# Kernel optimization log

Measured on AMD Instinct MI355X. Metric: run time of the kernel, lower is better.

The kernel has to match this reference:

```python
import jax, jax.numpy as jnp
import numpy as np

NBITS = 4
OUT_F = 2048
IN_F = 2048


def _bit_ste(w, nbits):
    # clamp to [-1,1], quantize magnitude to nbits levels, keep sign
    step = float(2 ** nbits - 1)
    w = jnp.clip(w, -1.0, 1.0)
    return jnp.round(jnp.abs(w) * step) / step * jnp.sign(w)


def setup_inputs() -> dict:
    key = jax.random.key(0)
    ks = jax.random.split(key, 6)
    ex = np.arange(NBITS - 1, -1, -1)
    exps = jnp.asarray(2.0 ** ex / (2.0 ** NBITS - 1), dtype=jnp.float32)
    inp = {
        "input": jax.random.normal(ks[0], (8, 2048, IN_F), dtype=jnp.float32),
        # bit-plane weights: sigmoid of these gives soft bits in (0,1)
        "pweight": jax.random.normal(ks[1], (OUT_F, IN_F, NBITS), dtype=jnp.float32),
        "nweight": jax.random.normal(ks[2], (OUT_F, IN_F, NBITS), dtype=jnp.float32),
        "exps": exps,
        "bexps": exps,
        "mask_weight": jnp.ones((NBITS,), dtype=jnp.float32),  # init.constant_(1)
        "scale": jnp.array([0.05], dtype=jnp.float32),
        "pbias": jax.random.uniform(ks[3], (OUT_F, NBITS), dtype=jnp.float32, minval=0.0, maxval=float(2 ** NBITS - 1)) // 1.0 % 2.0,
        "nbias": jax.random.uniform(ks[4], (OUT_F, NBITS), dtype=jnp.float32, minval=0.0, maxval=float(2 ** NBITS - 1)) // 1.0 % 2.0,
        "biasscale": jnp.array([0.05], dtype=jnp.float32),
    }
    return inp


def reference(input, pweight, nweight, exps, bexps, mask_weight, scale, pbias, nbias, biasscale):
    temp = 1.0
    # temp_s and mask_discrete are all-ones buffers -> identity factors
    mask = jax.nn.sigmoid(mask_weight)                      # [N]
    soft = jax.nn.sigmoid(temp * pweight) - jax.nn.sigmoid(temp * nweight)  # [O,I,N]
    weight = jnp.einsum('oin,n->oi', soft, exps * mask) * scale[0]          # [O,I]
    bias_raw = jnp.einsum('on,n->o', pbias - nbias, bexps)  # [O]
    bias = _bit_ste(bias_raw, NBITS) * biasscale[0]
    # F.linear: y = x @ W^T + b
    return jnp.einsum('bsi,oi->bso', input, weight) + bias
```

## Files before the change

kernel.cpp:

```cpp
#include <hip/hip_runtime.h>
#include <hip/hip_bf16.h>
#include <stdint.h>

#define M_DIM 16384
#define N_DIM 2048
#define K_DIM 2048

typedef __attribute__((ext_vector_type(8))) __bf16 bf16x8;
typedef __attribute__((ext_vector_type(4))) float f32x4;

__device__ __forceinline__ unsigned short f2bf(float f) {
  unsigned int u = __builtin_bit_cast(unsigned int, f);
  u += 0x7FFFu + ((u >> 16) & 1u);
  return (unsigned short)(u >> 16);
}

__device__ __forceinline__ float sigmoidf_(float x) {
  return 1.0f / (1.0f + __expf(-x));
}

__global__ __launch_bounds__(256) void convert_x(const float4* __restrict__ x,
                                                 uint4* __restrict__ xb) {
  int idx = blockIdx.x * 256 + threadIdx.x;
  float4 a = x[idx * 2];
  float4 b = x[idx * 2 + 1];
  uint4 r;
  r.x = (unsigned)f2bf(a.x) | ((unsigned)f2bf(a.y) << 16);
  r.y = (unsigned)f2bf(a.z) | ((unsigned)f2bf(a.w) << 16);
  r.z = (unsigned)f2bf(b.x) | ((unsigned)f2bf(b.y) << 16);
  r.w = (unsigned)f2bf(b.z) | ((unsigned)f2bf(b.w) << 16);
  xb[idx] = r;
}

__global__ __launch_bounds__(256) void make_w(const float4* __restrict__ pw,
                                              const float4* __restrict__ nw,
                                              const float* __restrict__ exps,
                                              const float* __restrict__ maskw,
                                              const float* __restrict__ scale,
                                              unsigned short* __restrict__ wout) {
  int idx = blockIdx.x * 256 + threadIdx.x;
  float4 p = pw[idx];
  float4 n = nw[idx];
  float s = scale[0];
  float c0 = sigmoidf_(maskw[0]) * exps[0] * s;
  float c1 = sigmoidf_(maskw[1]) * exps[1] * s;
  float c2 = sigmoidf_(maskw[2]) * exps[2] * s;
  float c3 = sigmoidf_(maskw[3]) * exps[3] * s;
  float w = (sigmoidf_(p.x) - sigmoidf_(n.x)) * c0
          + (sigmoidf_(p.y) - sigmoidf_(n.y)) * c1
          + (sigmoidf_(p.z) - sigmoidf_(n.z)) * c2
          + (sigmoidf_(p.w) - sigmoidf_(n.w)) * c3;
  wout[idx] = f2bf(w);
}

__global__ __launch_bounds__(256) void make_bias(const float* __restrict__ pb,
                                                 const float* __restrict__ nb,
                                                 const float* __restrict__ bexps,
                                                 const float* __restrict__ bscale,
                                                 float* __restrict__ bias) {
  int o = blockIdx.x * 256 + threadIdx.x;
  if (o < N_DIM) {
    float x = 0.f;
#pragma unroll
    for (int n = 0; n < 4; ++n) x += (pb[o * 4 + n] - nb[o * 4 + n]) * bexps[n];
    float xc = fminf(fmaxf(x, -1.f), 1.f);
    float mag = rintf(fabsf(xc) * 15.f) * (1.f / 15.f);
    float sgn = (xc > 0.f) ? 1.f : ((xc < 0.f) ? -1.f : 0.f);
    bias[o] = mag * sgn * bscale[0];
  }
}


#define BM 256
#define BN 256
#define BK 64
#define NT (K_DIM / BK)

__device__ __forceinline__ void gload16(const void* g, void* l) {
  __builtin_amdgcn_global_load_lds(
      (const __attribute__((address_space(1))) unsigned int*)g,
      (__attribute__((address_space(3))) unsigned int*)l, 16, 0, 0);
}

#define VMCNT(n) asm volatile("s_waitcnt vmcnt(" #n ")" ::: "memory")
#define BAR() __builtin_amdgcn_s_barrier()

__global__ __launch_bounds__(512, 2) void gemm_bias(const unsigned short* __restrict__ X,
                                                    const unsigned short* __restrict__ W,
                                                    const float* __restrict__ bias,
                                                    float* __restrict__ out) {
  __shared__ unsigned short sA[2][BM * BK];
  __shared__ unsigned short sB[2][BN * BK];

  const int tid = threadIdx.x;
  const int swz = ((int)blockIdx.x & 7) * 64 + ((int)blockIdx.x >> 3);
  const int bm = swz >> 3;
  const int bn = swz & 7;
  const int row0 = bm * BM, col0 = bn * BN;

  const int w = tid >> 6, l = tid & 63;
  const int wr = w >> 2;
  const int wc = w & 3;
  const int lr = l & 15;
  const int lk4 = l >> 4;
  const int l7 = l & 7;

  const unsigned short* Ag = X + (size_t)row0 * K_DIM;
  const unsigned short* Bg = W + (size_t)col0 * K_DIM;

  const int srl = (tid >> 3) & 31;
  const int sc16 = (tid & 7) ^ ((tid >> 3) & 7);
  const int shi = tid >> 8;
  const int slin = ((tid >> 3) & 24) * 64 + (tid & 63) * 8;

  auto stage = [&](unsigned short* lbase, const unsigned short* gbase,
                   int rb0, int rb1, int tk) {
    int rb = shi ? rb1 : rb0;
    int trow = rb + srl;
    gload16(gbase + (size_t)trow * K_DIM + tk * BK + sc16 * 8,
            lbase + rb * 64 + slin);
  };

  auto rdA = [&](const unsigned short* base, int mf, int ks) -> bf16x8 {
    int trow = wr * 128 + mf * 16 + lr;
    int c16l = (ks * 4 + lk4) ^ l7;
    return *(const bf16x8*)&base[trow * 64 + c16l * 8];
  };
  auto rdB = [&](const unsigned short* base, int nf, int ks) -> bf16x8 {
    int trow = wc * 64 + nf * 16 + lr;
    int c16l = (ks * 4 + lk4) ^ l7;
    return *(const bf16x8*)&base[trow * 64 + c16l * 8];
  };

  f32x4 acc[8][4] = {};
  bf16x8 a[4][2], b[4][2];

#define PHASE_MFMA(mh, nh)                                                    \
  __builtin_amdgcn_s_setprio(1);                                              \
  _Pragma("unroll") for (int i = 0; i < 4; ++i)                               \
  _Pragma("unroll") for (int j = 0; j < 2; ++j)                               \
  _Pragma("unroll") for (int ks = 0; ks < 2; ++ks)                            \
      acc[(mh) * 4 + i][(nh) * 2 + j] = __builtin_amdgcn_mfma_f32_16x16x32_bf16( \
          a[i][ks], b[(nh) * 2 + j][ks], acc[(mh) * 4 + i][(nh) * 2 + j], 0, 0, 0); \
  __builtin_amdgcn_s_setprio(0);

  {
    unsigned short* qa = sA[0];
    unsigned short* qb = sB[0];
    stage(qa, Ag, 0, 32, 0);
    stage(qa, Ag, 128, 160, 0);
    stage(qb, Bg, 0, 64, 0);
    stage(qb, Bg, 128, 192, 0);
    stage(qb, Bg, 32, 96, 0);
    stage(qb, Bg, 160, 224, 0);
    stage(qa, Ag, 64, 96, 0);
    stage(qa, Ag, 192, 224, 0);
  }
  VMCNT(4);
  BAR();

  for (int t = 0; t < NT; ++t) {
    const int p = t & 1, q = p ^ 1;
    const bool last = (t == NT - 1);
    const unsigned short* pa = sA[p];
    const unsigned short* pb = sB[p];
    unsigned short* qa = sA[q];
    unsigned short* qb = sB[q];

#pragma unroll
    for (int i = 0; i < 4; ++i)
#pragma unroll
      for (int ks = 0; ks < 2; ++ks) a[i][ks] = rdA(pa, i, ks);
#pragma unroll
    for (int j = 0; j < 2; ++j)
#pragma unroll
      for (int ks = 0; ks < 2; ++ks) b[j][ks] = rdB(pb, j, ks);
    if (!last) { stage(qa, Ag, 0, 32, t + 1); stage(qa, Ag, 128, 160, t + 1); }
    BAR();
    PHASE_MFMA(0, 0);
    if (!last) { VMCNT(4); } else { VMCNT(2); }
    BAR();

#pragma unroll
    for (int j = 2; j < 4; ++j)
#pragma unroll
      for (int ks = 0; ks < 2; ++ks) b[j][ks] = rdB(pb, j, ks);
    if (!last) { stage(qb, Bg, 0, 64, t + 1); stage(qb, Bg, 128, 192, t + 1); }
    BAR();
    PHASE_MFMA(0, 1);
    if (!last) { VMCNT(4); } else { VMCNT(0); }
    BAR();

#pragma unroll
    for (int i = 0; i < 4; ++i)
#pragma unroll
      for (int ks = 0; ks < 2; ++ks) a[i][ks] = rdA(pa, 4 + i, ks);
    if (!last) { stage(qb, Bg, 32, 96, t + 1); stage(qb, Bg, 160, 224, t + 1); }
    BAR();
    PHASE_MFMA(1, 0);
    BAR();

    if (!last) { stage(qa, Ag, 64, 96, t + 1); stage(qa, Ag, 192, 224, t + 1); }
    BAR();
    PHASE_MFMA(1, 1);
    if (!last) { VMCNT(4); }
    BAR();
  }

  float bv[4];
#pragma unroll
  for (int nf = 0; nf < 4; ++nf) bv[nf] = bias[col0 + wc * 64 + nf * 16 + lr];
  const int orow = lk4 * 4;
#pragma unroll
  for (int mf = 0; mf < 8; ++mf) {
#pragma unroll
    for (int nf = 0; nf < 4; ++nf) {
      const int colg = col0 + wc * 64 + nf * 16 + lr;
#pragma unroll
      for (int r = 0; r < 4; ++r) {
        int rowg = row0 + wr * 128 + mf * 16 + orow + r;
        out[(size_t)rowg * N_DIM + colg] = acc[mf][nf][r] + bv[nf];
      }
    }
  }
#undef PHASE_MFMA
}

extern "C" void kernel_launch(void* const* d_in, const int* in_sizes, int n_in,
                              void* d_out, int out_size, void* d_ws, size_t ws_size,
                              hipStream_t stream) {
  const float* input  = (const float*)d_in[0];
  const float* pweight = (const float*)d_in[1];
  const float* nweight = (const float*)d_in[2];
  const float* exps   = (const float*)d_in[3];
  const float* bexps  = (const float*)d_in[4];
  const float* maskw  = (const float*)d_in[5];
  const float* scale  = (const float*)d_in[6];
  const float* pbias  = (const float*)d_in[7];
  const float* nbias  = (const float*)d_in[8];
  const float* bscale = (const float*)d_in[9];
  float* out = (float*)d_out;

  unsigned short* Xb = (unsigned short*)d_ws;
  unsigned short* Wb = (unsigned short*)((char*)d_ws + (size_t)M_DIM * K_DIM * 2);
  float* bias = (float*)((char*)d_ws + (size_t)M_DIM * K_DIM * 2 + (size_t)N_DIM * K_DIM * 2);

  convert_x<<<(M_DIM * (size_t)K_DIM) / 8 / 256, 256, 0, stream>>>((const float4*)input, (uint4*)Xb);
  make_w<<<((size_t)N_DIM * K_DIM) / 256, 256, 0, stream>>>(
      (const float4*)pweight, (const float4*)nweight, exps, maskw, scale, Wb);
  make_bias<<<(N_DIM + 255) / 256, 256, 0, stream>>>(pbias, nbias, bexps, bscale, bias);

  dim3 grid((M_DIM / BM) * (N_DIM / BN));
  gemm_bias<<<grid, 512, 0, stream>>>(Xb, Wb, bias, out);
}
```

Baseline: 205.3 us.

## Deepen GEMM prefetch to stage half of tile t+2 during iteration t

Restructures the double-buffered LDS pipeline so the prologue loads tile 0 plus half of tile 1. Each iteration then issues the remaining half of t+1 early and the first half of t+2 into the buffer just consumed. This keeps more global loads in flight across iterations, aiming to hide memory latency behind the MFMA phases. Wrapped tile indices let the last iterations issue redundant loads instead of branching. The vmcnt waits are re-tuned to match, which risks ordering errors or redundant traffic.

```diff
diff --git a/kernel.cpp b/kernel.cpp
--- a/kernel.cpp
+++ b/kernel.cpp
@@ -144,28 +144,27 @@
           a[i][ks], b[(nh) * 2 + j][ks], acc[(mh) * 4 + i][(nh) * 2 + j], 0, 0, 0); \
   __builtin_amdgcn_s_setprio(0);
 
-  {
-    unsigned short* qa = sA[0];
-    unsigned short* qb = sB[0];
-    stage(qa, Ag, 0, 32, 0);
-    stage(qa, Ag, 128, 160, 0);
-    stage(qb, Bg, 0, 64, 0);
-    stage(qb, Bg, 128, 192, 0);
-    stage(qb, Bg, 32, 96, 0);
-    stage(qb, Bg, 160, 224, 0);
-    stage(qa, Ag, 64, 96, 0);
-    stage(qa, Ag, 192, 224, 0);
-  }
-  VMCNT(4);
+  stage(sA[0], Ag, 0, 32, 0);
+  stage(sA[0], Ag, 128, 160, 0);
+  stage(sB[0], Bg, 0, 64, 0);
+  stage(sB[0], Bg, 128, 192, 0);
+  stage(sB[0], Bg, 32, 96, 0);
+  stage(sB[0], Bg, 160, 224, 0);
+  stage(sA[0], Ag, 64, 96, 0);
+  stage(sA[0], Ag, 192, 224, 0);
+  stage(sA[1], Ag, 0, 32, 1);
+  stage(sA[1], Ag, 128, 160, 1);
+  stage(sB[1], Bg, 0, 64, 1);
+  stage(sB[1], Bg, 128, 192, 1);
+  VMCNT(8);
   BAR();
 
   for (int t = 0; t < NT; ++t) {
     const int p = t & 1, q = p ^ 1;
-    const bool last = (t == NT - 1);
+    const int t1 = (t + 1) & (NT - 1);
+    const int t2 = (t + 2) & (NT - 1);
     const unsigned short* pa = sA[p];
     const unsigned short* pb = sB[p];
-    unsigned short* qa = sA[q];
-    unsigned short* qb = sB[q];
 
 #pragma unroll
     for (int i = 0; i < 4; ++i)
@@ -175,35 +174,39 @@
     for (int j = 0; j < 2; ++j)
 #pragma unroll
       for (int ks = 0; ks < 2; ++ks) b[j][ks] = rdB(pb, j, ks);
-    if (!last) { stage(qa, Ag, 0, 32, t + 1); stage(qa, Ag, 128, 160, t + 1); }
+    stage(sB[q], Bg, 32, 96, t1);
+    stage(sB[q], Bg, 160, 224, t1);
+    stage(sA[q], Ag, 64, 96, t1);
+    stage(sA[q], Ag, 192, 224, t1);
     BAR();
     PHASE_MFMA(0, 0);
-    if (!last) { VMCNT(4); } else { VMCNT(2); }
+    VMCNT(10);
     BAR();
 
 #pragma unroll
     for (int j = 2; j < 4; ++j)
 #pragma unroll
       for (int ks = 0; ks < 2; ++ks) b[j][ks] = rdB(pb, j, ks);
-    if (!last) { stage(qb, Bg, 0, 64, t + 1); stage(qb, Bg, 128, 192, t + 1); }
     BAR();
     PHASE_MFMA(0, 1);
-    if (!last) { VMCNT(4); } else { VMCNT(0); }
+    VMCNT(8);
     BAR();
 
 #pragma unroll
     for (int i = 0; i < 4; ++i)
 #pragma unroll
       for (int ks = 0; ks < 2; ++ks) a[i][ks] = rdA(pa, 4 + i, ks);
-    if (!last) { stage(qb, Bg, 32, 96, t + 1); stage(qb, Bg, 160, 224, t + 1); }
     BAR();
     PHASE_MFMA(1, 0);
     BAR();
 
-    if (!last) { stage(qa, Ag, 64, 96, t + 1); stage(qa, Ag, 192, 224, t + 1); }
+    stage(sA[p], Ag, 0, 32, t2);
+    stage(sA[p], Ag, 128, 160, t2);
+    stage(sB[p], Bg, 0, 64, t2);
+    stage(sB[p], Bg, 128, 192, t2);
     BAR();
     PHASE_MFMA(1, 1);
-    if (!last) { VMCNT(4); }
+    VMCNT(8);
     BAR();
   }
 
```

After: 223.0 us. 8.6% more time.
